# Optimization experiments

Measured on AMD Instinct MI355X. Metric: run time of the kernel, lower is better.

The kernel has to match this reference:

```python
import jax, jax.numpy as jnp
import numpy as np

SEQ, BATCH, EMB = 512, 1024, 100
HID, D_FF, D_OUT = 6, 200, 2


def setup_inputs() -> dict:
    key = jax.random.key(0)
    ks = jax.random.split(key, 14)
    s_in = 1.0 / np.sqrt(HID)  # torch nn.RNN init scale
    inp = {
        "x": jax.random.normal(ks[0], (SEQ, BATCH, EMB), dtype=jnp.float32),
        # layer 0 (input_size=EMB -> hidden=6)
        "W_ih0": jax.random.uniform(ks[1], (HID, EMB), jnp.float32, -s_in, s_in),
        "W_hh0": jax.random.uniform(ks[2], (HID, HID), jnp.float32, -s_in, s_in),
        "b_ih0": jax.random.uniform(ks[3], (HID,), jnp.float32, -s_in, s_in),
        "b_hh0": jax.random.uniform(ks[4], (HID,), jnp.float32, -s_in, s_in),
        # layer 1 (hidden=6 -> hidden=6)
        "W_ih1": jax.random.uniform(ks[5], (HID, HID), jnp.float32, -s_in, s_in),
        "W_hh1": jax.random.uniform(ks[6], (HID, HID), jnp.float32, -s_in, s_in),
        "b_ih1": jax.random.uniform(ks[7], (HID,), jnp.float32, -s_in, s_in),
        "b_hh1": jax.random.uniform(ks[8], (HID,), jnp.float32, -s_in, s_in),
        # MLP head: Linear(6, 200) then Linear(200, 2)
        "W1": jax.random.uniform(ks[9], (D_FF, HID), jnp.float32, -s_in, s_in),
        "b1": jax.random.uniform(ks[10], (D_FF,), jnp.float32, -s_in, s_in),
        "W2": jax.random.uniform(ks[11], (D_OUT, D_FF), jnp.float32, -1.0 / np.sqrt(D_FF), 1.0 / np.sqrt(D_FF)),
        "b2": jax.random.uniform(ks[12], (D_OUT,), jnp.float32, -1.0 / np.sqrt(D_FF), 1.0 / np.sqrt(D_FF)),
    }
    return inp


def _rnn_forward(x, W_ih0, W_hh0, b_ih0, b_hh0, W_ih1, W_hh1, b_ih1, b_hh1):
    # Precompute the big input projection for layer 0 in one GEMM: [S,B,H]
    pre0 = jnp.einsum('sbe,he->sbh', x, W_ih0) + (b_ih0 + b_hh0)
    h0_init = jnp.zeros((x.shape[1], HID), x.dtype)
    h1_init = jnp.zeros((x.shape[1], HID), x.dtype)

    def step(carry, p0_t):
        h0, h1 = carry
        h0 = jax.nn.relu(p0_t + h0 @ W_hh0.T)
        h1 = jax.nn.relu(h0 @ W_ih1.T + b_ih1 + h1 @ W_hh1.T + b_hh1)
        return (h0, h1), None

    (h0_T, h1_T), _ = jax.lax.scan(step, (h0_init, h1_init), pre0)
    return h1_T  # == output[-1] of the 2-layer RNN, shape [B, H]


def reference(x, W_ih0, W_hh0, b_ih0, b_hh0, W_ih1, W_hh1, b_ih1, b_hh1, W1, b1, W2, b2):
    last = _rnn_forward(x, W_ih0, W_hh0, b_ih0, b_hh0, W_ih1, W_hh1, b_ih1, b_hh1)
    h = last @ W1.T + b1          # [B, 200]
    out = h @ W2.T + b2           # [B, 2]
    return out
```

## Files before the change

kernel.cpp:

```cpp
#include <hip/hip_runtime.h>

#define SEQ 512
#define BATCH 1024
#define EMB 100
#define HID 6
#define DFF 200
#define SB (SEQ*BATCH)

__global__ __launch_bounds__(64) void pre0_kernel(
    const float* __restrict__ x, const float* __restrict__ Wih0,
    const float* __restrict__ bih0, const float* __restrict__ bhh0,
    float* __restrict__ pre0)
{
    __shared__ float4 xlds[64*25];
    __shared__ float4 wlds[6*25];
    __shared__ float  blds[8];

    const int lane = threadIdx.x;
    const int rowbase = blockIdx.x * 64;

    const float4* __restrict__ wg4 = (const float4*)Wih0;
    #pragma unroll
    for (int k = 0; k < 3; k++){
        int i = lane + 64*k;
        if (i < 150) wlds[i] = wg4[i];
    }
    if (lane < 6) blds[lane] = bih0[lane] + bhh0[lane];

    const float4* __restrict__ x4 = (const float4*)x;
    const size_t gbase = (size_t)rowbase * 25;
    #pragma unroll
    for (int k = 0; k < 25; k++)
        xlds[lane + 64*k] = x4[gbase + lane + 64*k];

    __syncthreads();

    float acc[6];
    #pragma unroll
    for (int h = 0; h < 6; h++) acc[h] = blds[h];

    #pragma unroll
    for (int c = 0; c < 25; c++){
        const float4 xv = xlds[lane*25 + c];
        #pragma unroll
        for (int h = 0; h < 6; h++){
            const float4 wv = wlds[h*25 + c];
            acc[h] += xv.x*wv.x;
            acc[h] += xv.y*wv.y;
            acc[h] += xv.z*wv.z;
            acc[h] += xv.w*wv.w;
        }
    }

    float4* __restrict__ p4 = (float4*)pre0;
    const int row = rowbase + lane;
    p4[row*2+0] = make_float4(acc[0],acc[1],acc[2],acc[3]);
    p4[row*2+1] = make_float4(acc[4],acc[5],0.f,0.f);
}

__global__ __launch_bounds__(64) void scan_kernel(
    const float* __restrict__ pre0,
    const float* __restrict__ Whh0, const float* __restrict__ Wih1,
    const float* __restrict__ Whh1, const float* __restrict__ bih1,
    const float* __restrict__ bhh1,
    const float* __restrict__ W1, const float* __restrict__ b1v,
    const float* __restrict__ W2, const float* __restrict__ b2v,
    float* __restrict__ out)
{
    const int b = blockIdx.x*64 + threadIdx.x;

    float whh0[36], wih1[36], whh1[36], bias1[6];
    #pragma unroll
    for (int i=0;i<36;i++) whh0[i]=Whh0[i];
    #pragma unroll
    for (int i=0;i<36;i++) wih1[i]=Wih1[i];
    #pragma unroll
    for (int i=0;i<36;i++) whh1[i]=Whh1[i];
    #pragma unroll
    for (int h=0;h<6;h++) bias1[h]=bih1[h]+bhh1[h];

    float h0[6]={0,0,0,0,0,0}, h1[6]={0,0,0,0,0,0};

    const float4* __restrict__ p4 = (const float4*)pre0;

    float4 pf0[4], pf1[4];
    #pragma unroll
    for (int k=0;k<4;k++){
        const int r = k*BATCH + b;
        pf0[k] = p4[r*2+0];
        pf1[k] = p4[r*2+1];
    }

    for (int s=0; s<SEQ; s+=4){
        #pragma unroll
        for (int u=0;u<4;u++){
            const float4 c0 = pf0[u], c1 = pf1[u];
            const int ns = s + u + 4;
            if (ns < SEQ){
                const int r = ns*BATCH + b;
                pf0[u] = p4[r*2+0];
                pf1[u] = p4[r*2+1];
            }
            const float p[6] = {c0.x,c0.y,c0.z,c0.w,c1.x,c1.y};

            float h0n[6];
            #pragma unroll
            for (int h=0;h<6;h++){
                float a = p[h];
                #pragma unroll
                for (int j=0;j<6;j++) a += whh0[h*6+j]*h0[j];
                h0n[h] = fmaxf(a, 0.f);
            }
            float h1n[6];
            #pragma unroll
            for (int h=0;h<6;h++){
                float a = bias1[h];
                #pragma unroll
                for (int j=0;j<6;j++) a += wih1[h*6+j]*h0n[j];
                #pragma unroll
                for (int j=0;j<6;j++) a += whh1[h*6+j]*h1[j];
                h1n[h] = fmaxf(a, 0.f);
            }
            #pragma unroll
            for (int h=0;h<6;h++){ h0[h]=h0n[h]; h1[h]=h1n[h]; }
        }
    }

    float o0 = b2v[0], o1 = b2v[1];
    for (int f=0; f<DFF; f++){
        float hf = b1v[f];
        #pragma unroll
        for (int h=0;h<6;h++) hf += W1[f*6+h]*h1[h];
        o0 += W2[f]*hf;
        o1 += W2[DFF+f]*hf;
    }
    out[b*2+0]=o0; out[b*2+1]=o1;
}

extern "C" void kernel_launch(void* const* d_in, const int* in_sizes, int n_in,
                              void* d_out, int out_size, void* d_ws, size_t ws_size,
                              hipStream_t stream)
{
    const float* x    = (const float*)d_in[0];
    const float* Wih0 = (const float*)d_in[1];
    const float* Whh0 = (const float*)d_in[2];
    const float* bih0 = (const float*)d_in[3];
    const float* bhh0 = (const float*)d_in[4];
    const float* Wih1 = (const float*)d_in[5];
    const float* Whh1 = (const float*)d_in[6];
    const float* bih1 = (const float*)d_in[7];
    const float* bhh1 = (const float*)d_in[8];
    const float* W1   = (const float*)d_in[9];
    const float* b1v  = (const float*)d_in[10];
    const float* W2   = (const float*)d_in[11];
    const float* b2v  = (const float*)d_in[12];
    float* out  = (float*)d_out;
    float* pre0 = (float*)d_ws;

    pre0_kernel<<<SB/64, 64, 0, stream>>>(x, Wih0, bih0, bhh0, pre0);
    scan_kernel<<<BATCH/64, 64, 0, stream>>>(pre0, Whh0, Wih1, Whh1, bih1, bhh1,
                                             W1, b1v, W2, b2v, out);
}
```

Measured before the change: 562.5 us.

## Use direct global-to-LDS loads and deeper asm-prefetched scan pipeline

In the projection kernel, x tiles are loaded with the global_load_lds builtin, which writes straight into LDS and skips the register round-trip. In the scan kernel, the software prefetch of pre0 timesteps grows from 4 to 8 steps. It uses inline-asm global loads with explicit vmcnt waits and sched barriers, so each step only waits on its own oldest load. The goal is to hide global memory latency in the latency-bound serial recurrence, at the cost of fragile hand-managed waitcnt ordering and extra registers.

Result: faster. 540.6 us (-3.9%).

```diff
diff --git a/kernel.cpp b/kernel.cpp
--- a/kernel.cpp
+++ b/kernel.cpp
@@ -6,6 +6,9 @@
 #define HID 6
 #define DFF 200
 #define SB (SEQ*BATCH)
+
+typedef __attribute__((address_space(1))) void gvoid;
+typedef __attribute__((address_space(3))) void lvoid;
 
 __global__ __launch_bounds__(64) void pre0_kernel(
     const float* __restrict__ x, const float* __restrict__ Wih0,
@@ -19,6 +22,14 @@
     const int lane = threadIdx.x;
     const int rowbase = blockIdx.x * 64;
 
+    const float4* __restrict__ x4 = (const float4*)x;
+    const size_t gbase = (size_t)rowbase * 25;
+    #pragma unroll
+    for (int k = 0; k < 25; k++){
+        const float4* gp = x4 + gbase + lane + 64*k;
+        __builtin_amdgcn_global_load_lds((gvoid*)gp, (lvoid*)&xlds[64*k], 16, 0, 0);
+    }
+
     const float4* __restrict__ wg4 = (const float4*)Wih0;
     #pragma unroll
     for (int k = 0; k < 3; k++){
@@ -26,12 +37,6 @@
         if (i < 150) wlds[i] = wg4[i];
     }
     if (lane < 6) blds[lane] = bih0[lane] + bhh0[lane];
-
-    const float4* __restrict__ x4 = (const float4*)x;
-    const size_t gbase = (size_t)rowbase * 25;
-    #pragma unroll
-    for (int k = 0; k < 25; k++)
-        xlds[lane + 64*k] = x4[gbase + lane + 64*k];
 
     __syncthreads();
 
@@ -83,48 +88,62 @@
 
     const float4* __restrict__ p4 = (const float4*)pre0;
 
-    float4 pf0[4], pf1[4];
+    auto step = [&](const float4& c0, const float4& c1){
+        const float p[6] = {c0.x,c0.y,c0.z,c0.w,c1.x,c1.y};
+        float h0n[6];
+        #pragma unroll
+        for (int h=0;h<6;h++){
+            float a = p[h];
+            #pragma unroll
+            for (int j=0;j<6;j++) a += whh0[h*6+j]*h0[j];
+            h0n[h] = fmaxf(a, 0.f);
+        }
+        float h1n[6];
+        #pragma unroll
+        for (int h=0;h<6;h++){
+            float a = bias1[h];
+            #pragma unroll
+            for (int j=0;j<6;j++) a += wih1[h*6+j]*h0n[j];
+            #pragma unroll
+            for (int j=0;j<6;j++) a += whh1[h*6+j]*h1[j];
+            h1n[h] = fmaxf(a, 0.f);
+        }
+        #pragma unroll
+        for (int h=0;h<6;h++){ h0[h]=h0n[h]; h1[h]=h1n[h]; }
+    };
+
+    float4 r0[8], r1[8];
+
     #pragma unroll
-    for (int k=0;k<4;k++){
-        const int r = k*BATCH + b;
-        pf0[k] = p4[r*2+0];
-        pf1[k] = p4[r*2+1];
+    for (int k=0;k<8;k++){
+        const float4* a = p4 + ((size_t)(k*BATCH + b))*2;
+        asm volatile("global_load_dwordx4 %0, %2, off\n\t"
+                     "global_load_dwordx4 %1, %2, off offset:16"
+                     : "=&v"(r0[k]), "=&v"(r1[k])
+                     : "v"(a)
+                     : "memory");
     }
 
-    for (int s=0; s<SEQ; s+=4){
+    for (int s=0; s<SEQ-8; s+=8){
         #pragma unroll
-        for (int u=0;u<4;u++){
-            const float4 c0 = pf0[u], c1 = pf1[u];
-            const int ns = s + u + 4;
-            if (ns < SEQ){
-                const int r = ns*BATCH + b;
-                pf0[u] = p4[r*2+0];
-                pf1[u] = p4[r*2+1];
-            }
-            const float p[6] = {c0.x,c0.y,c0.z,c0.w,c1.x,c1.y};
-
-            float h0n[6];
-            #pragma unroll
-            for (int h=0;h<6;h++){
-                float a = p[h];
-                #pragma unroll
-                for (int j=0;j<6;j++) a += whh0[h*6+j]*h0[j];
-                h0n[h] = fmaxf(a, 0.f);
-            }
-            float h1n[6];
-            #pragma unroll
-            for (int h=0;h<6;h++){
-                float a = bias1[h];
-                #pragma unroll
-                for (int j=0;j<6;j++) a += wih1[h*6+j]*h0n[j];
-                #pragma unroll
-                for (int j=0;j<6;j++) a += whh1[h*6+j]*h1[j];
-                h1n[h] = fmaxf(a, 0.f);
-            }
-            #pragma unroll
-            for (int h=0;h<6;h++){ h0[h]=h0n[h]; h1[h]=h1n[h]; }
+        for (int u=0;u<8;u++){
+            asm volatile("s_waitcnt vmcnt(14)" ::: "memory");
+            __builtin_amdgcn_sched_barrier(0);
+            const float4 c0 = r0[u], c1 = r1[u];
+            step(c0, c1);
+            const float4* a = p4 + ((size_t)((s+u+8)*BATCH + b))*2;
+            asm volatile("global_load_dwordx4 %0, %2, off\n\t"
+                         "global_load_dwordx4 %1, %2, off offset:16"
+                         : "=&v"(r0[u]), "=&v"(r1[u])
+                         : "v"(a)
+                         : "memory");
         }
     }
+
+    asm volatile("s_waitcnt vmcnt(0)" ::: "memory");
+    __builtin_amdgcn_sched_barrier(0);
+    #pragma unroll
+    for (int u=0;u<8;u++) step(r0[u], r1[u]);
 
     float o0 = b2v[0], o1 = b2v[1];
     for (int f=0; f<DFF; f++){
```
